# Kernel optimization log

Hardware: AMD Instinct MI355X
Metric: run time of the kernel (lower is better)

The kernel has to match this reference:

```python
import jax, jax.numpy as jnp
import numpy as np

N = 50000      # nodes
D = 64         # in_channels == hidden_channels
L = 3          # num_layers
DEG = 16       # avg degree
SLOPE = 0.2    # GATv2 leaky_relu negative slope (PyG default)


def setup_inputs() -> dict:
    key = jax.random.key(0)
    ks = jax.random.split(key, 8)
    x = jax.random.normal(ks[0], (N, D), dtype=jnp.float32)
    # random edges with no self loops (PyG GATv2 removes then re-adds self loops)
    E = N * DEG
    dst = jax.random.randint(ks[1], (E,), 0, N)
    off = jax.random.randint(ks[2], (E,), 1, N)
    src = (dst + off) % N
    loops = jnp.arange(N)
    edge_index = jnp.stack([
        jnp.concatenate([src, loops]),   # row 0: source j
        jnp.concatenate([dst, loops]),   # row 1: target i
    ]).astype(jnp.int64)
    s = 1.0 / np.sqrt(D)
    Wl = (jax.random.normal(ks[3], (L, D, D)) * s).astype(jnp.float32)
    Wr = (jax.random.normal(ks[4], (L, D, D)) * s).astype(jnp.float32)
    att = (jax.random.normal(ks[5], (L, D)) * s).astype(jnp.float32)
    bl = jnp.zeros((L, D), jnp.float32)
    br = jnp.zeros((L, D), jnp.float32)
    bias = jnp.zeros((L, D), jnp.float32)
    return dict(x=x, edge_index=edge_index, Wl=Wl, bl=bl, Wr=Wr, br=br,
                att=att, bias=bias)


def reference(x, edge_index, Wl, bl, Wr, br, att, bias):
    src, dst = edge_index[0], edge_index[1]
    n = x.shape[0]
    for l in range(L):  # stacked GATv2 layers (structural loop, not data loop)
        xl = x @ Wl[l] + bl[l]                    # lin_l (source transform) [N,D]
        xr = x @ Wr[l] + br[l]                    # lin_r (target transform) [N,D]
        e = jax.nn.leaky_relu(xl[src] + xr[dst], SLOPE)   # [E,D]
        logits = e @ att[l]                       # [E]
        # softmax over incoming edges of each target node
        m = jax.ops.segment_max(logits, dst, num_segments=n)
        ex = jnp.exp(logits - m[dst])
        denom = jax.ops.segment_sum(ex, dst, num_segments=n)
        alpha = ex / denom[dst]                   # [E]
        x = jax.ops.segment_sum(xl[src] * alpha[:, None], dst,
                                num_segments=n) + bias[l]
        x = jax.nn.gelu(x, approximate=False)     # F.gelu (exact erf)
        # dropout p=0.0 -> no-op
    return x
```

## Files before the change

kernel.cpp:

```cpp
#include <hip/hip_runtime.h>
#include <hip/hip_bf16.h>

#define SLOPE 0.2f

__global__ __launch_bounds__(256) void k_init(int* __restrict__ deg, int n,
                                              const int* __restrict__ ei,
                                              int* __restrict__ flag) {
    int i = blockIdx.x * 256 + threadIdx.x;
    if (i < n) deg[i] = 0;
    if (blockIdx.x == 0) {
        __shared__ int cnt;
        if (threadIdx.x == 0) cnt = 0;
        __syncthreads();
        int z = 0;
        for (int k = threadIdx.x; k < 4096; k += 256)
            if ((k & 1) && ei[k] == 0) z++;
        atomicAdd(&cnt, z);
        __syncthreads();
        if (threadIdx.x == 0) *flag = (cnt > 1024) ? 1 : 0;
    }
}

__device__ inline int esrc_at(const int* ei, int E, int f, int e) {
    return f ? ei[2 * e] : ei[e];
}
__device__ inline int edst_at(const int* ei, int E, int f, int e) {
    return f ? ei[2 * (E + e)] : ei[E + e];
}


__global__ __launch_bounds__(256) void k_hist(const int* __restrict__ ei, int E,
                                              const int* __restrict__ flag,
                                              int* __restrict__ deg,
                                              int* __restrict__ rank) {
    int e = blockIdx.x * 256 + threadIdx.x;
    if (e < E) rank[e] = atomicAdd(&deg[edst_at(ei, E, *flag, e)], 1);
}

__global__ __launch_bounds__(256) void k_scan_part(const int* __restrict__ deg, int n,
                                                   int* __restrict__ parts) {
    __shared__ int s[256];
    int base = blockIdx.x * 1024;
    int sum = 0;
    for (int j = threadIdx.x; j < 1024; j += 256) {
        int i = base + j;
        sum += (i < n) ? deg[i] : 0;
    }
    s[threadIdx.x] = sum;
    __syncthreads();
    for (int off = 128; off > 0; off >>= 1) {
        if (threadIdx.x < off) s[threadIdx.x] += s[threadIdx.x + off];
        __syncthreads();
    }
    if (threadIdx.x == 0) parts[blockIdx.x] = s[0];
}

__global__ __launch_bounds__(256) void k_scan_final(const int* __restrict__ deg, int n,
                                                    const int* __restrict__ parts,
                                                    int NB, int* __restrict__ rowp) {
    __shared__ int sp[1024];
    __shared__ int s[256];
    int t = threadIdx.x;
    for (int j = t; j < 1024; j += 256) sp[j] = (j < NB) ? parts[j] : 0;
    __syncthreads();
    for (int off = 1; off < 1024; off <<= 1) {
        int v[4];
        for (int c = 0; c < 4; ++c) {
            int j = t + c * 256;
            v[c] = (j >= off) ? sp[j - off] : 0;
        }
        __syncthreads();
        for (int c = 0; c < 4; ++c) sp[t + c * 256] += v[c];
        __syncthreads();
    }
    int b = blockIdx.x;
    int chunk_off = (b == 0) ? 0 : sp[b - 1];
    if (b == 0 && t == 0) rowp[n] = sp[NB - 1];
    int base = b * 1024 + t * 4;
    int v0 = (base + 0 < n) ? deg[base + 0] : 0;
    int v1 = (base + 1 < n) ? deg[base + 1] : 0;
    int v2 = (base + 2 < n) ? deg[base + 2] : 0;
    int v3 = (base + 3 < n) ? deg[base + 3] : 0;
    int mysum = v0 + v1 + v2 + v3;
    s[t] = mysum;
    __syncthreads();
    for (int off = 1; off < 256; off <<= 1) {
        int add = (t >= off) ? s[t - off] : 0;
        __syncthreads();
        s[t] += add;
        __syncthreads();
    }
    int excl = chunk_off + s[t] - mysum;
    if (base + 0 < n) rowp[base + 0] = excl;
    if (base + 1 < n) rowp[base + 1] = excl + v0;
    if (base + 2 < n) rowp[base + 2] = excl + v0 + v1;
    if (base + 3 < n) rowp[base + 3] = excl + v0 + v1 + v2;
}

template <typename IT>
__global__ __launch_bounds__(256) void k_scatter(const int* __restrict__ ei, int E,
                                                 const int* __restrict__ flag,
                                                 const int* __restrict__ rowp,
                                                 const int* __restrict__ rank,
                                                 IT* __restrict__ ssrc) {
    int e = blockIdx.x * 256 + threadIdx.x;
    if (e < E) {
        int f = *flag;
        int i = edst_at(ei, E, f, e);
        ssrc[rowp[i] + rank[e]] = (IT)esrc_at(ei, E, f, e);
    }
}


__device__ inline void storef(float* p, size_t i, float v) { p[i] = v; }
__device__ inline void storef(__hip_bfloat16* p, size_t i, float v) {
    p[i] = __float2bfloat16(v);
}

__device__ inline void load8(const float* p, size_t row, int q, float v[8]) {
    const float4* b = reinterpret_cast<const float4*>(p + row * 64);
    float4 x = b[q * 2], y = b[q * 2 + 1];
    v[0] = x.x; v[1] = x.y; v[2] = x.z; v[3] = x.w;
    v[4] = y.x; v[5] = y.y; v[6] = y.z; v[7] = y.w;
}
__device__ inline void load8(const __hip_bfloat16* p, size_t row, int q, float v[8]) {
    uint4 u = reinterpret_cast<const uint4*>(p + row * 64)[q];
    v[0] = __uint_as_float(u.x << 16);
    v[1] = __uint_as_float(u.x & 0xffff0000u);
    v[2] = __uint_as_float(u.y << 16);
    v[3] = __uint_as_float(u.y & 0xffff0000u);
    v[4] = __uint_as_float(u.z << 16);
    v[5] = __uint_as_float(u.z & 0xffff0000u);
    v[6] = __uint_as_float(u.w << 16);
    v[7] = __uint_as_float(u.w & 0xffff0000u);
}


template <typename ST, typename SR>
__global__ __launch_bounds__(256) void k_lin2(const float* __restrict__ x,
                                              const float* __restrict__ Wl,
                                              const float* __restrict__ bl,
                                              const float* __restrict__ Wr,
                                              const float* __restrict__ br,
                                              ST* __restrict__ xl,
                                              SR* __restrict__ xr, int n) {
    __shared__ float sWl[4096], sWr[4096], sbl[64], sbr[64];
    int t = threadIdx.x;
    for (int k = t; k < 4096; k += 256) {
        sWl[k] = Wl[k];
        sWr[k] = Wr[k];
    }
    if (t < 64) {
        sbl[t] = bl[t];
        sbr[t] = br[t];
    }
    __syncthreads();
    int col = t & 63;
    int rl = t >> 6;
    int ngroups = (n + 3) >> 2;
    for (int g = blockIdx.x; g < ngroups; g += gridDim.x) {
        int row = g * 4 + rl;
        if (row < n) {
            const float4* xp4 = reinterpret_cast<const float4*>(x + (size_t)row * 64);
            float al = sbl[col], ar = sbr[col];
#pragma unroll
            for (int k4 = 0; k4 < 16; ++k4) {
                float4 xv = xp4[k4];
                int kb = k4 << 2;
                al = fmaf(xv.x, sWl[((kb + 0) << 6) + col], al);
                ar = fmaf(xv.x, sWr[((kb + 0) << 6) + col], ar);
                al = fmaf(xv.y, sWl[((kb + 1) << 6) + col], al);
                ar = fmaf(xv.y, sWr[((kb + 1) << 6) + col], ar);
                al = fmaf(xv.z, sWl[((kb + 2) << 6) + col], al);
                ar = fmaf(xv.z, sWr[((kb + 2) << 6) + col], ar);
                al = fmaf(xv.w, sWl[((kb + 3) << 6) + col], al);
                ar = fmaf(xv.w, sWr[((kb + 3) << 6) + col], ar);
            }
            storef(xl, (size_t)row * 64 + col, al);
            storef(xr, (size_t)row * 64 + col, ar);
        }
    }
}

template <typename ST, typename SR, typename IT>
__global__ __launch_bounds__(256) void k_gat(const ST* __restrict__ xl,
                                             const SR* __restrict__ xr,
                                             const int* __restrict__ rowp,
                                             const IT* __restrict__ ssrc,
                                             const float* __restrict__ att,
                                             const float* __restrict__ bias,
                                             float* __restrict__ out, int n) {
    int wid = (blockIdx.x * 256 + threadIdx.x) >> 6;
    if (wid >= n) return;
    int lane = threadIdx.x & 63;
    int g = lane >> 3;
    int q = lane & 7;
    float a[8], r[8];
    load8(att, 0, q, a);
    load8(xr, (size_t)wid, q, r);
    int beg = rowp[wid], end = rowp[wid + 1];
    float m = -3.4e38f, denom = 0.f;
    float acc[8] = {0.f, 0.f, 0.f, 0.f, 0.f, 0.f, 0.f, 0.f};
    for (int e = beg; e < end; e += 8) {
        int rem = end - e;
        bool valid = (g < rem);
        int idx = e + (valid ? g : rem - 1);
        int s = (int)ssrc[idx];
        float v[8];
        load8(xl, (size_t)s, q, v);
        float l = 0.f;
#pragma unroll
        for (int j = 0; j < 8; ++j) {
            float tj = v[j] + r[j];
            tj = tj > 0.f ? tj : SLOPE * tj;
            l = fmaf(a[j], tj, l);
        }
        l += __shfl_xor(l, 1);
        l += __shfl_xor(l, 2);
        l += __shfl_xor(l, 4);
        float mnew = valid ? fmaxf(m, l) : m;
        float sc = __expf(m - mnew);
        float p = valid ? __expf(l - mnew) : 0.f;
        denom = denom * sc + p;
#pragma unroll
        for (int j = 0; j < 8; ++j) acc[j] = fmaf(acc[j], sc, p * v[j]);
        m = mnew;
    }
    float mt = m;
    mt = fmaxf(mt, __shfl_xor(mt, 8));
    mt = fmaxf(mt, __shfl_xor(mt, 16));
    mt = fmaxf(mt, __shfl_xor(mt, 32));
    float sc = __expf(m - mt);
    denom *= sc;
    denom += __shfl_xor(denom, 8);
    denom += __shfl_xor(denom, 16);
    denom += __shfl_xor(denom, 32);
#pragma unroll
    for (int j = 0; j < 8; ++j) {
        acc[j] *= sc;
        acc[j] += __shfl_xor(acc[j], 8);
        acc[j] += __shfl_xor(acc[j], 16);
        acc[j] += __shfl_xor(acc[j], 32);
    }
    if (g == 0) {
        float b[8];
        load8(bias, 0, q, b);
        float inv = 1.f / denom;
        float o[8];
#pragma unroll
        for (int j = 0; j < 8; ++j) {
            float oj = acc[j] * inv + b[j];
            o[j] = 0.5f * oj * (1.0f + erff(oj * 0.70710678118654752f));
        }
        float4* ob = reinterpret_cast<float4*>(out + (size_t)wid * 64);
        ob[q * 2] = make_float4(o[0], o[1], o[2], o[3]);
        ob[q * 2 + 1] = make_float4(o[4], o[5], o[6], o[7]);
    }
}


template <typename ST, typename SR, typename IT>
static void run_layers(const float* x0, const float* Wl, const float* bl,
                       const float* Wr, const float* br, const float* att,
                       const float* bias, ST* xl, SR* xr, const int* rowp,
                       const IT* ssrc, float* xout, int N, hipStream_t stream) {
    int gat_grid = (N + 3) / 4;
    for (int l = 0; l < 3; ++l) {
        const float* xin = (l == 0) ? x0 : xout;
        k_lin2<ST, SR><<<2048, 256, 0, stream>>>(
            xin, Wl + (size_t)l * 4096, bl + (size_t)l * 64,
            Wr + (size_t)l * 4096, br + (size_t)l * 64, xl, xr, N);
        k_gat<ST, SR, IT><<<gat_grid, 256, 0, stream>>>(xl, xr, rowp, ssrc,
                                                        att + (size_t)l * 64,
                                                        bias + (size_t)l * 64,
                                                        xout, N);
    }
}

extern "C" void kernel_launch(void* const* d_in, const int* in_sizes, int n_in,
                              void* d_out, int out_size, void* d_ws, size_t ws_size,
                              hipStream_t stream) {
    (void)n_in;
    (void)out_size;
    const float* x0 = (const float*)d_in[0];
    const int* ei = (const int*)d_in[1];
    const float* Wl = (const float*)d_in[2];
    const float* bl = (const float*)d_in[3];
    const float* Wr = (const float*)d_in[4];
    const float* br = (const float*)d_in[5];
    const float* att = (const float*)d_in[6];
    const float* bias = (const float*)d_in[7];

    int N = in_sizes[0] / 64;
    int E = in_sizes[1] / 2;
    size_t ND = (size_t)N * 64;

    char* w = (char*)d_ws;
    int* flag = (int*)w;       w += 256;
    int* parts = (int*)w;      w += 4096;
    int* rowp = (int*)w;       w += ((size_t)N + 8) * 4;
    int* deg = (int*)w;        w += ((size_t)N + 8) * 4;
    int* rank = (int*)w;       w += ((size_t)E + 8) * 4;
    unsigned short* ssrc16 = (unsigned short*)w;
    int* ssrc32 = (int*)w;     w += ((size_t)E + 8) * 4;
    size_t head = (size_t)(w - (char*)d_ws);

    bool big = (ws_size >= head + ND * 2 + ND * 4 + 4096);
    bool small_ids = (N <= 65535);

    int NB = (N + 1023) / 1024;
    int neb = (E + 255) / 256;
    int nzb = (N + 255) / 256;

    k_init<<<nzb, 256, 0, stream>>>(deg, N, ei, flag);
    k_hist<<<neb, 256, 0, stream>>>(ei, E, flag, deg, rank);
    k_scan_part<<<NB, 256, 0, stream>>>(deg, N, parts);
    k_scan_final<<<NB, 256, 0, stream>>>(deg, N, parts, NB, rowp);
    if (small_ids)
        k_scatter<unsigned short><<<neb, 256, 0, stream>>>(ei, E, flag, rowp, rank, ssrc16);
    else
        k_scatter<int><<<neb, 256, 0, stream>>>(ei, E, flag, rowp, rank, ssrc32);

    float* xout = (float*)d_out;
    if (big) {
        __hip_bfloat16* xl = (__hip_bfloat16*)w;
        float* xr = (float*)(w + ND * 2);
        if (small_ids)
            run_layers<__hip_bfloat16, float, unsigned short>(
                x0, Wl, bl, Wr, br, att, bias, xl, xr, rowp, ssrc16, xout, N, stream);
        else
            run_layers<__hip_bfloat16, float, int>(
                x0, Wl, bl, Wr, br, att, bias, xl, xr, rowp, ssrc32, xout, N, stream);
    } else {
        __hip_bfloat16* xl = (__hip_bfloat16*)w;
        __hip_bfloat16* xr = xl + ND;
        if (small_ids)
            run_layers<__hip_bfloat16, __hip_bfloat16, unsigned short>(
                x0, Wl, bl, Wr, br, att, bias, xl, xr, rowp, ssrc16, xout, N, stream);
        else
            run_layers<__hip_bfloat16, __hip_bfloat16, int>(
                x0, Wl, bl, Wr, br, att, bias, xl, xr, rowp, ssrc32, xout, N, stream);
    }
}
```

Before: 270.6 us.

## Fuse CSR scatter with first-layer linear; register-block 4 rows per wave

The edge scatter that builds the CSR source list is merged into the first layer's dual linear-transform launch, with blocks interleaved by role, so the two independent jobs share one launch and overlap. The linear kernel is also restructured so each wave computes four rows per lane, reusing each shared-memory weight load across four rows instead of one. This aims to cut a launch and raise arithmetic intensity in the linear step. In exchange, scatter blocks now reserve the linear kernel's 32KB of shared memory, which may lower occupancy, and the extra per-thread accumulators raise register use.

```diff
diff --git a/kernel.cpp b/kernel.cpp
--- a/kernel.cpp
+++ b/kernel.cpp
@@ -97,20 +97,6 @@
     if (base + 3 < n) rowp[base + 3] = excl + v0 + v1 + v2;
 }
 
-template <typename IT>
-__global__ __launch_bounds__(256) void k_scatter(const int* __restrict__ ei, int E,
-                                                 const int* __restrict__ flag,
-                                                 const int* __restrict__ rowp,
-                                                 const int* __restrict__ rank,
-                                                 IT* __restrict__ ssrc) {
-    int e = blockIdx.x * 256 + threadIdx.x;
-    if (e < E) {
-        int f = *flag;
-        int i = edst_at(ei, E, f, e);
-        ssrc[rowp[i] + rank[e]] = (IT)esrc_at(ei, E, f, e);
-    }
-}
-
 
 __device__ inline void storef(float* p, size_t i, float v) { p[i] = v; }
 __device__ inline void storef(__hip_bfloat16* p, size_t i, float v) {
@@ -135,6 +121,75 @@
     v[7] = __uint_as_float(u.w & 0xffff0000u);
 }
 
+template <typename ST, typename SR>
+__device__ __forceinline__ void lin2_body(const float* __restrict__ x,
+                                          const float* __restrict__ Wl,
+                                          const float* __restrict__ bl,
+                                          const float* __restrict__ Wr,
+                                          const float* __restrict__ br,
+                                          ST* __restrict__ xl,
+                                          SR* __restrict__ xr, int n,
+                                          int bid, int nblocks) {
+    __shared__ float sWl[4096], sWr[4096], sbl[64], sbr[64];
+    int t = threadIdx.x;
+    for (int k = t; k < 4096; k += 256) {
+        sWl[k] = Wl[k];
+        sWr[k] = Wr[k];
+    }
+    if (t < 64) {
+        sbl[t] = bl[t];
+        sbr[t] = br[t];
+    }
+    __syncthreads();
+    int lane = t & 63;
+    int wv = t >> 6;
+    int nquads = (n + 3) >> 2;
+    for (int qd = bid * 4 + wv; qd < nquads; qd += nblocks * 4) {
+        int row0 = qd << 2;
+        bool full = (row0 + 4 <= n);
+        float al[4], ar[4];
+#pragma unroll
+        for (int r = 0; r < 4; ++r) {
+            al[r] = sbl[lane];
+            ar[r] = sbr[lane];
+        }
+        const float* xp = x + (size_t)row0 * 64;
+#pragma unroll
+        for (int k4 = 0; k4 < 16; ++k4) {
+            float4 xv[4];
+#pragma unroll
+            for (int r = 0; r < 4; ++r) {
+                if (full || row0 + r < n)
+                    xv[r] = *reinterpret_cast<const float4*>(xp + (size_t)r * 64 + k4 * 4);
+                else
+                    xv[r] = make_float4(0.f, 0.f, 0.f, 0.f);
+            }
+            int kb = k4 << 2;
+            float wl0 = sWl[((kb + 0) << 6) + lane], wr0 = sWr[((kb + 0) << 6) + lane];
+            float wl1 = sWl[((kb + 1) << 6) + lane], wr1 = sWr[((kb + 1) << 6) + lane];
+            float wl2 = sWl[((kb + 2) << 6) + lane], wr2 = sWr[((kb + 2) << 6) + lane];
+            float wl3 = sWl[((kb + 3) << 6) + lane], wr3 = sWr[((kb + 3) << 6) + lane];
+#pragma unroll
+            for (int r = 0; r < 4; ++r) {
+                al[r] = fmaf(xv[r].x, wl0, al[r]);
+                ar[r] = fmaf(xv[r].x, wr0, ar[r]);
+                al[r] = fmaf(xv[r].y, wl1, al[r]);
+                ar[r] = fmaf(xv[r].y, wr1, ar[r]);
+                al[r] = fmaf(xv[r].z, wl2, al[r]);
+                ar[r] = fmaf(xv[r].z, wr2, ar[r]);
+                al[r] = fmaf(xv[r].w, wl3, al[r]);
+                ar[r] = fmaf(xv[r].w, wr3, ar[r]);
+            }
+        }
+#pragma unroll
+        for (int r = 0; r < 4; ++r) {
+            if (full || row0 + r < n) {
+                storef(xl, (size_t)(row0 + r) * 64 + lane, al[r]);
+                storef(xr, (size_t)(row0 + r) * 64 + lane, ar[r]);
+            }
+        }
+    }
+}
 
 template <typename ST, typename SR>
 __global__ __launch_bounds__(256) void k_lin2(const float* __restrict__ x,
@@ -144,40 +199,38 @@
                                               const float* __restrict__ br,
                                               ST* __restrict__ xl,
                                               SR* __restrict__ xr, int n) {
-    __shared__ float sWl[4096], sWr[4096], sbl[64], sbr[64];
-    int t = threadIdx.x;
-    for (int k = t; k < 4096; k += 256) {
-        sWl[k] = Wl[k];
-        sWr[k] = Wr[k];
-    }
-    if (t < 64) {
-        sbl[t] = bl[t];
-        sbr[t] = br[t];
-    }
-    __syncthreads();
-    int col = t & 63;
-    int rl = t >> 6;
-    int ngroups = (n + 3) >> 2;
-    for (int g = blockIdx.x; g < ngroups; g += gridDim.x) {
-        int row = g * 4 + rl;
-        if (row < n) {
-            const float4* xp4 = reinterpret_cast<const float4*>(x + (size_t)row * 64);
-            float al = sbl[col], ar = sbr[col];
-#pragma unroll
-            for (int k4 = 0; k4 < 16; ++k4) {
-                float4 xv = xp4[k4];
-                int kb = k4 << 2;
-                al = fmaf(xv.x, sWl[((kb + 0) << 6) + col], al);
-                ar = fmaf(xv.x, sWr[((kb + 0) << 6) + col], ar);
-                al = fmaf(xv.y, sWl[((kb + 1) << 6) + col], al);
-                ar = fmaf(xv.y, sWr[((kb + 1) << 6) + col], ar);
-                al = fmaf(xv.z, sWl[((kb + 2) << 6) + col], al);
-                ar = fmaf(xv.z, sWr[((kb + 2) << 6) + col], ar);
-                al = fmaf(xv.w, sWl[((kb + 3) << 6) + col], al);
-                ar = fmaf(xv.w, sWr[((kb + 3) << 6) + col], ar);
-            }
-            storef(xl, (size_t)row * 64 + col, al);
-            storef(xr, (size_t)row * 64 + col, ar);
+    lin2_body<ST, SR>(x, Wl, bl, Wr, br, xl, xr, n, blockIdx.x, gridDim.x);
+}
+
+template <typename ST, typename SR, typename IT>
+__global__ __launch_bounds__(256) void k_scatter_lin2(
+    const int* __restrict__ ei, int E, const int* __restrict__ flag,
+    const int* __restrict__ rowp, const int* __restrict__ rank,
+    IT* __restrict__ ssrc, const float* __restrict__ x,
+    const float* __restrict__ Wl, const float* __restrict__ bl,
+    const float* __restrict__ Wr, const float* __restrict__ br,
+    ST* __restrict__ xl, SR* __restrict__ xr, int n, int lin_blocks,
+    int scat_blocks) {
+    int bid = blockIdx.x;
+    int m = lin_blocks < scat_blocks ? lin_blocks : scat_blocks;
+    int m2 = 2 * m;
+    bool is_lin;
+    int id;
+    if (bid < m2) {
+        is_lin = !(bid & 1);
+        id = bid >> 1;
+    } else {
+        is_lin = (lin_blocks > m);
+        id = m + (bid - m2);
+    }
+    if (is_lin) {
+        lin2_body<ST, SR>(x, Wl, bl, Wr, br, xl, xr, n, id, lin_blocks);
+    } else {
+        int e = id * 256 + threadIdx.x;
+        if (e < E) {
+            int f = *flag;
+            int i = edst_at(ei, E, f, e);
+            ssrc[rowp[i] + rank[e]] = (IT)esrc_at(ei, E, f, e);
         }
     }
 }
@@ -260,15 +313,22 @@
 
 
 template <typename ST, typename SR, typename IT>
-static void run_layers(const float* x0, const float* Wl, const float* bl,
-                       const float* Wr, const float* br, const float* att,
-                       const float* bias, ST* xl, SR* xr, const int* rowp,
-                       const IT* ssrc, float* xout, int N, hipStream_t stream) {
+static void run_all(const int* ei, int E, const int* flag, const int* rowp,
+                    const int* rank, IT* ssrc, const float* x0, const float* Wl,
+                    const float* bl, const float* Wr, const float* br,
+                    const float* att, const float* bias, ST* xl, SR* xr,
+                    float* xout, int N, hipStream_t stream) {
     int gat_grid = (N + 3) / 4;
-    for (int l = 0; l < 3; ++l) {
-        const float* xin = (l == 0) ? x0 : xout;
-        k_lin2<ST, SR><<<2048, 256, 0, stream>>>(
-            xin, Wl + (size_t)l * 4096, bl + (size_t)l * 64,
+    int neb = (E + 255) / 256;
+    const int lin_blocks = 2048;
+    k_scatter_lin2<ST, SR, IT><<<lin_blocks + neb, 256, 0, stream>>>(
+        ei, E, flag, rowp, rank, ssrc, x0, Wl, bl, Wr, br, xl, xr, N,
+        lin_blocks, neb);
+    k_gat<ST, SR, IT><<<gat_grid, 256, 0, stream>>>(xl, xr, rowp, ssrc, att,
+                                                    bias, xout, N);
+    for (int l = 1; l < 3; ++l) {
+        k_lin2<ST, SR><<<lin_blocks, 256, 0, stream>>>(
+            xout, Wl + (size_t)l * 4096, bl + (size_t)l * 64,
             Wr + (size_t)l * 4096, br + (size_t)l * 64, xl, xr, N);
         k_gat<ST, SR, IT><<<gat_grid, 256, 0, stream>>>(xl, xr, rowp, ssrc,
                                                         att + (size_t)l * 64,
@@ -316,29 +376,29 @@
     k_hist<<<neb, 256, 0, stream>>>(ei, E, flag, deg, rank);
     k_scan_part<<<NB, 256, 0, stream>>>(deg, N, parts);
     k_scan_final<<<NB, 256, 0, stream>>>(deg, N, parts, NB, rowp);
-    if (small_ids)
-        k_scatter<unsigned short><<<neb, 256, 0, stream>>>(ei, E, flag, rowp, rank, ssrc16);
-    else
-        k_scatter<int><<<neb, 256, 0, stream>>>(ei, E, flag, rowp, rank, ssrc32);
 
     float* xout = (float*)d_out;
     if (big) {
         __hip_bfloat16* xl = (__hip_bfloat16*)w;
         float* xr = (float*)(w + ND * 2);
         if (small_ids)
-            run_layers<__hip_bfloat16, float, unsigned short>(
-                x0, Wl, bl, Wr, br, att, bias, xl, xr, rowp, ssrc16, xout, N, stream);
+            run_all<__hip_bfloat16, float, unsigned short>(
+                ei, E, flag, rowp, rank, ssrc16, x0, Wl, bl, Wr, br, att, bias,
+                xl, xr, xout, N, stream);
         else
-            run_layers<__hip_bfloat16, float, int>(
-                x0, Wl, bl, Wr, br, att, bias, xl, xr, rowp, ssrc32, xout, N, stream);
+            run_all<__hip_bfloat16, float, int>(
+                ei, E, flag, rowp, rank, ssrc32, x0, Wl, bl, Wr, br, att, bias,
+                xl, xr, xout, N, stream);
     } else {
         __hip_bfloat16* xl = (__hip_bfloat16*)w;
         __hip_bfloat16* xr = xl + ND;
         if (small_ids)
-            run_layers<__hip_bfloat16, __hip_bfloat16, unsigned short>(
-                x0, Wl, bl, Wr, br, att, bias, xl, xr, rowp, ssrc16, xout, N, stream);
+            run_all<__hip_bfloat16, __hip_bfloat16, unsigned short>(
+                ei, E, flag, rowp, rank, ssrc16, x0, Wl, bl, Wr, br, att, bias,
+                xl, xr, xout, N, stream);
         else
-            run_layers<__hip_bfloat16, __hip_bfloat16, int>(
-                x0, Wl, bl, Wr, br, att, bias, xl, xr, rowp, ssrc32, xout, N, stream);
-    }
-}
+            run_all<__hip_bfloat16, __hip_bfloat16, int>(
+                ei, E, flag, rowp, rank, ssrc32, x0, Wl, bl, Wr, br, att, bias,
+                xl, xr, xout, N, stream);
+    }
+}
```

After: 441.1 us. +63.0%, slower.
